# Optimization experiments

Hardware: AMD Instinct MI355X
Metric: run time of the kernel (lower is better)

Reference implementation:

```python
import jax, jax.numpy as jnp
import numpy as np

B, L, A, D = 4, 512, 8, 256
H = 256  # hidden_dim
O = 256  # output_dim


def setup_inputs() -> dict:
    key = jax.random.key(0)
    ks = jax.random.split(key, 12)
    s = 0.05
    return {
        "x": jax.random.normal(ks[0], (B, L, A, D), dtype=jnp.float32),
        "conv_w": jax.random.normal(ks[1], (H, D), dtype=jnp.float32) * s,
        "conv_b": jax.random.normal(ks[2], (H,), dtype=jnp.float32) * s,
        "theta_w": jax.random.normal(ks[3], (H, H), dtype=jnp.float32) * s,
        "theta_b": jax.random.normal(ks[4], (H,), dtype=jnp.float32) * s,
        "phi_w": jax.random.normal(ks[5], (H, H), dtype=jnp.float32) * s,
        "phi_b": jax.random.normal(ks[6], (H,), dtype=jnp.float32) * s,
        "g_w": jax.random.normal(ks[7], (H, H), dtype=jnp.float32) * s,
        "g_b": jax.random.normal(ks[8], (H,), dtype=jnp.float32) * s,
        "f_w": jax.random.normal(ks[9], (O, H), dtype=jnp.float32) * s,
        "f_b": jax.random.normal(ks[10], (O,), dtype=jnp.float32) * s,
    }


def reference(x, conv_w, conv_b, theta_w, theta_b, phi_w, phi_b, g_w, g_b, f_w, f_b):
    batch, length, n_agents, _ = x.shape
    # residual: identity (input_dim == output_dim, stride 1)
    res = x
    # conv with kernel (1,1): pointwise projection over channel dim
    h = jnp.einsum('blad,hd->blah', x, conv_w) + conv_b  # [B,L,A,H]
    N = length * n_agents
    h = h.reshape(batch, N, H)
    theta = jnp.einsum('bnh,kh->bnk', h, theta_w) + theta_b  # [B,N,H]
    phi = jnp.einsum('bnh,kh->bnk', h, phi_w) + phi_b        # [B,N,H]
    g = jnp.einsum('bnh,kh->bnk', h, g_w) + g_b              # [B,N,H]
    scores = jnp.einsum('bnk,bmk->bnm', theta, phi) / jnp.sqrt(jnp.asarray(H, theta.dtype))
    y = jax.nn.softmax(scores, axis=2)                       # [B,N,N]
    z = jnp.einsum('bnm,bmk->bnk', y, g) / jnp.sqrt(jnp.asarray(N, y.dtype))
    out = jnp.einsum('bnk,ok->bno', z, f_w) + f_b            # [B,N,O]
    out = out.reshape(batch, length, n_agents, O)
    return out + res
```

## Files before the change

kernel.cpp:

```cpp
#include <hip/hip_runtime.h>

typedef unsigned short u16;
typedef __bf16 bf16x8 __attribute__((ext_vector_type(8)));
typedef float f32x4 __attribute__((ext_vector_type(4)));
typedef float f32x16 __attribute__((ext_vector_type(16)));
typedef float float4v __attribute__((ext_vector_type(4)));
typedef unsigned short u16x8 __attribute__((ext_vector_type(8)));
typedef unsigned short u16x4 __attribute__((ext_vector_type(4)));

#define MFMA16(a, b, c) __builtin_amdgcn_mfma_f32_16x16x32_bf16(a, b, c, 0, 0, 0)
#define MFMA32(a, b, c) __builtin_amdgcn_mfma_f32_32x32x16_bf16(a, b, c, 0, 0, 0)

__device__ __forceinline__ u16 f2bf(float f) {
  union { float f; unsigned u; } v; v.f = f;
  unsigned r = v.u + 0x7fffu + ((v.u >> 16) & 1u);
  return (u16)(r >> 16);
}
__device__ __forceinline__ float bf2f(u16 b) {
  union { unsigned u; float f; } v; v.u = ((unsigned)b) << 16;
  return v.f;
}

__device__ __forceinline__ void gload16(const void* g, void* l) {
  __builtin_amdgcn_global_load_lds(
      (__attribute__((address_space(1))) void*)g,
      (__attribute__((address_space(3))) void*)l, 16, 0, 0);
}

__device__ __forceinline__ unsigned cvtpk(float lo, float hi) {
  unsigned r;
  asm("v_cvt_pk_bf16_f32 %0, %1, %2" : "=v"(r) : "v"(lo), "v"(hi));
  return r;
}
__device__ __forceinline__ void plswap(unsigned& a, unsigned& b) {
  asm volatile("v_permlane32_swap_b32 %0, %1" : "+v"(a), "+v"(b));
}

__global__ __launch_bounds__(256) void prep_all(
    const float* __restrict__ cw, const float* __restrict__ tw,
    const float* __restrict__ pw, const float* __restrict__ gw,
    const float* __restrict__ fw,
    const float* __restrict__ cb, const float* __restrict__ tb,
    const float* __restrict__ pb, const float* __restrict__ gb,
    u16* __restrict__ Wbig, float* __restrict__ biasp) {
  const int t = threadIdx.x;
  const int bid = blockIdx.x;
  const int n3 = bid & 255;
  __shared__ float w3s[256];
  __shared__ float us[256];
  __shared__ float red[4];
  float pv;
  if (bid < 512) {
    const float* wsrc = bid < 256 ? tw : pw;
    w3s[t] = wsrc[(size_t)n3 * 256 + t];
    __syncthreads();
    float acc = 0.0f;
#pragma unroll 8
    for (int h = 0; h < 256; ++h) acc = fmaf(w3s[h], cw[(size_t)h * 256 + t], acc);
    Wbig[(size_t)bid * 256 + t] = f2bf(acc);
    pv = w3s[t] * cb[t];
  } else {
    w3s[t] = fw[(size_t)n3 * 256 + t];
    __syncthreads();
    float u = 0.0f;
#pragma unroll 8
    for (int h = 0; h < 256; ++h) u = fmaf(w3s[h], gw[(size_t)h * 256 + t], u);
    us[t] = u;
    __syncthreads();
    float acc = 0.0f;
#pragma unroll 8
    for (int k = 0; k < 256; ++k) acc = fmaf(us[k], cw[(size_t)k * 256 + t], acc);
    Wbig[(size_t)bid * 256 + t] = f2bf(acc);
    pv = us[t] * cb[t] + w3s[t] * gb[t];
  }
#pragma unroll
  for (int m = 1; m < 64; m <<= 1) pv += __shfl_xor(pv, m, 64);
  if ((t & 63) == 0) red[t >> 6] = pv;
  __syncthreads();
  if (t == 0) {
    float d = red[0] + red[1] + red[2] + red[3];
    biasp[bid] = d + (bid < 256 ? tb[n3] : bid < 512 ? pb[n3] : 0.0f);
  }
}

__global__ __launch_bounds__(256) void gemm_tpg(
    const float* __restrict__ X, const u16* __restrict__ W,
    const float* __restrict__ bias, u16* __restrict__ tpg,
    u16* __restrict__ gT) {
  __shared__ u16 S[16384];
  u16* As = S;
  u16* Bs = S + 8192;
  const int t = threadIdx.x;
  const int lane = t & 63, w = t >> 6;
  const int brow = blockIdx.x * 128, bcol = blockIdx.y * 128;
  const int wr = (w >> 1) * 64, wc = (w & 1) * 64;
  f32x4 acc[4][4];
#pragma unroll
  for (int i = 0; i < 4; ++i)
#pragma unroll
    for (int j = 0; j < 4; ++j)
#pragma unroll
      for (int r = 0; r < 4; ++r) acc[i][j][r] = 0.0f;

  const int sr = t >> 3, sc8 = (t & 7) * 8;
  const u16* gW = W + (size_t)(bcol + sr) * 256 + sc8;
  const int ar = t & 127, ach = t >> 7;
  const float* gX = X + (size_t)(brow + ar) * 256 + ach * 32;

  for (int kt = 0; kt < 256; kt += 64) {
#pragma unroll
    for (int c = 0; c < 4; ++c)
      gload16(gW + (size_t)c * 32 * 256 + kt, &Bs[c * 2048 + t * 8]);
    u16x8 pk[4];
#pragma unroll
    for (int j = 0; j < 4; ++j) {
      float4v v0 = *(const float4v*)(gX + kt + j * 8);
      float4v v1 = *(const float4v*)(gX + kt + j * 8 + 4);
#pragma unroll
      for (int e = 0; e < 4; ++e) { pk[j][e] = f2bf(v0[e]); pk[j][4 + e] = f2bf(v1[e]); }
    }
#pragma unroll
    for (int j = 0; j < 4; ++j) {
      int unit = (ach * 4 + j) ^ (ar & 7);
      *(u16x8*)(&As[ar * 64 + unit * 8]) = pk[j];
    }
    __syncthreads();
#pragma unroll
    for (int kk = 0; kk < 2; ++kk) {
      const int ko = kk * 32 + (lane >> 4) * 8;
      bf16x8 af[4], bfr[4];
#pragma unroll
      for (int i = 0; i < 4; ++i) {
        int R = wr + i * 16 + (lane & 15);
        int unit = (kk * 4 + (lane >> 4)) ^ (R & 7);
        af[i] = *(const bf16x8*)(&As[R * 64 + unit * 8]);
      }
#pragma unroll
      for (int j = 0; j < 4; ++j)
        bfr[j] = *(const bf16x8*)(&Bs[(wc + j * 16 + (lane & 15)) * 64 + ko]);
#pragma unroll
      for (int i = 0; i < 4; ++i)
#pragma unroll
        for (int j = 0; j < 4; ++j)
          acc[i][j] = MFMA16(af[i], bfr[j], acc[i][j]);
    }
    __syncthreads();
  }

  const int r0 = (lane >> 4) * 4, c0 = lane & 15;
  if (blockIdx.y < 4) {
#pragma unroll
    for (int i = 0; i < 4; ++i)
#pragma unroll
      for (int j = 0; j < 4; ++j) {
        const int col = bcol + wc + j * 16 + c0;
        const float bv = bias[col];
#pragma unroll
        for (int r = 0; r < 4; ++r) {
          const size_t o = (size_t)(brow + wr + i * 16 + r0 + r) * 512 + col;
          tpg[o] = f2bf(acc[i][j][r] + bv);
        }
      }
  } else {
    const int vcb = bcol - 512;
    const int b = brow >> 12, n0 = brow & 4095;
#pragma unroll
    for (int h = 0; h < 2; ++h) {
      if (wr == h * 64) {
#pragma unroll
        for (int i = 0; i < 4; ++i)
#pragma unroll
          for (int j = 0; j < 4; ++j) {
            const int col = wc + j * 16 + c0;
            const float bv = bias[bcol + col];
            const int rowl = i * 16 + r0;
            u16x4 ov;
#pragma unroll
            for (int r = 0; r < 4; ++r) ov[r] = f2bf(acc[i][j][r] + bv);
            *(u16x4*)(&S[col * 72 + rowl]) = ov;
          }
      }
      __syncthreads();
#pragma unroll
      for (int k = 0; k < 4; ++k) {
        const int col = k * 32 + (t >> 3);
        const int mch = (t & 7) * 8;
        u16x8 v = *(const u16x8*)(&S[col * 72 + mch]);
        *(u16x8*)(&gT[((size_t)((b << 8) + vcb + col)) * 4096 + n0 + h * 64 + mch]) = v;
      }
      __syncthreads();
    }
  }
}

__global__ __launch_bounds__(256, 2) void flash2(
    const u16* __restrict__ tpg, const u16* __restrict__ gT,
    u16* __restrict__ Zp, u16* __restrict__ Lpb) {
  __shared__ u16 Kl[2][32 * 256];
  __shared__ u16 Vl[2][256 * 32];

  const int t = threadIdx.x;
  const int lane = t & 63, w = t >> 6;
  const int l31 = lane & 31, hi = lane >> 5;
  const int bid = blockIdx.x;
  const int b = bid >> 7;
  const int quarter = (bid >> 5) & 3;
  const int qt = bid & 31;
  const int q0 = qt * 128 + w * 32;
  const int kv0 = quarter * 1024;

  bf16x8 q[16];
  {
    const u16* qp = tpg + (size_t)(b * 4096 + q0 + l31) * 512 + hi * 8;
#pragma unroll
    for (int ks = 0; ks < 16; ++ks) q[ks] = *(const bf16x8*)(qp + ks * 16);
  }

  f32x16 zacc[8];
#pragma unroll
  for (int i = 0; i < 8; ++i)
#pragma unroll
    for (int j = 0; j < 16; ++j) zacc[i][j] = 0.0f;
  float ell = 0.0f;

  const int ksr = t >> 5, ksc = t & 31;

  auto stage = [&](int tile, int bi) {
    const size_t krow0 = (size_t)(b * 4096 + kv0 + tile * 32);
#pragma unroll
    for (int ch = 0; ch < 4; ++ch) {
      int r = ch * 8 + ksr;
      gload16(tpg + (krow0 + r) * 512 + 256 + ((ksc ^ r) * 8), &Kl[bi][ch * 2048 + t * 8]);
    }
#pragma unroll
    for (int ch = 0; ch < 4; ++ch) {
      int u = ch * 256 + t;
      int r = u >> 2, c16 = u & 3;
      gload16(gT + (size_t)(b * 256 + r) * 4096 + kv0 + tile * 32 + ((c16 ^ ((r >> 1) & 3)) * 8),
              &Vl[bi][u * 8]);
    }
  };

  stage(0, 0);
  __syncthreads();

  for (int tile = 0; tile < 32; ++tile) {
    const int cur = tile & 1;
    if (tile + 1 < 32) stage(tile + 1, cur ^ 1);

    f32x16 s;
#pragma unroll
    for (int j = 0; j < 16; ++j) s[j] = 0.0f;
    const u16* kb = &Kl[cur][0];
    __builtin_amdgcn_s_setprio(1);
#pragma unroll
    for (int ks = 0; ks < 16; ++ks) {
      bf16x8 kf = *(const bf16x8*)(kb + l31 * 256 + (((2 * ks + hi) ^ l31) * 8));
      s = MFMA32(kf, q[ks], s);
    }
    __builtin_amdgcn_s_setprio(0);

    bf16x8 pa[2];
#pragma unroll
    for (int half = 0; half < 2; ++half) {
      float p[8];
#pragma unroll
      for (int g = 0; g < 8; ++g) {
        p[g] = __builtin_amdgcn_exp2f(s[half * 8 + g] * 0.09016844f);
        ell += p[g];
      }
      unsigned x0 = cvtpk(p[0], p[1]), y0 = cvtpk(p[4], p[5]);
      unsigned x1 = cvtpk(p[2], p[3]), y1 = cvtpk(p[6], p[7]);
      plswap(x0, y0);
      plswap(x1, y1);
      union { unsigned u[4]; bf16x8 v; } cc;
      cc.u[0] = x0; cc.u[1] = x1; cc.u[2] = y0; cc.u[3] = y1;
      pa[half] = cc.v;
    }

    const u16* vb = &Vl[cur][0];
    __builtin_amdgcn_s_setprio(1);
#pragma unroll
    for (int ks2 = 0; ks2 < 2; ++ks2) {
#pragma unroll
      for (int nt = 0; nt < 8; ++nt) {
        int row = nt * 32 + l31;
        bf16x8 vv = *(const bf16x8*)(vb + row * 32 + (((2 * ks2 + hi) ^ ((row >> 1) & 3)) * 8));
        zacc[nt] = MFMA32(pa[ks2], vv, zacc[nt]);
      }
    }
    __builtin_amdgcn_s_setprio(0);
    __syncthreads();
  }

  ell += __shfl_xor(ell, 32, 64);

#pragma unroll
  for (int g = 0; g < 16; ++g) {
    int r = (g & 3) + 8 * (g >> 2) + 4 * hi;
    size_t rowoff = ((size_t)(quarter * 16384 + b * 4096 + q0 + r)) * 256 + l31;
#pragma unroll
    for (int nt = 0; nt < 8; ++nt) Zp[rowoff + nt * 32] = f2bf(zacc[nt][g]);
  }
  if (lane < 32) Lpb[quarter * 16384 + b * 4096 + q0 + l31] = f2bf(ell);
}

__global__ __launch_bounds__(256) void merge_out(
    const u16* __restrict__ Zp, const u16* __restrict__ Lpb,
    const float* __restrict__ fb, const float* __restrict__ x,
    float* __restrict__ out) {
  const int idx = blockIdx.x * 256 + threadIdx.x;
  const int m = idx >> 5;
  const int c = (idx & 31) * 8;
  const float l = bf2f(Lpb[m]) + bf2f(Lpb[16384 + m]) + bf2f(Lpb[32768 + m]) +
                  bf2f(Lpb[49152 + m]);
  const float inv = 1.0f / (l * 64.0f);
  float acc[8];
#pragma unroll
  for (int j = 0; j < 8; ++j) acc[j] = 0.0f;
#pragma unroll
  for (int qd = 0; qd < 4; ++qd) {
    u16x8 v = *(const u16x8*)(Zp + ((size_t)(qd * 16384) + m) * 256 + c);
#pragma unroll
    for (int j = 0; j < 8; ++j) acc[j] += bf2f(v[j]);
  }
  const float4v fb0 = *(const float4v*)(fb + c);
  const float4v fb1 = *(const float4v*)(fb + c + 4);
  const float4v x0 = *(const float4v*)(x + (size_t)m * 256 + c);
  const float4v x1 = *(const float4v*)(x + (size_t)m * 256 + c + 4);
  float4v o0, o1;
#pragma unroll
  for (int j = 0; j < 4; ++j) {
    o0[j] = acc[j] * inv + fb0[j] + x0[j];
    o1[j] = acc[4 + j] * inv + fb1[j] + x1[j];
  }
  *(float4v*)(out + (size_t)m * 256 + c) = o0;
  *(float4v*)(out + (size_t)m * 256 + c + 4) = o1;
}

extern "C" void kernel_launch(void* const* d_in, const int* in_sizes, int n_in,
                              void* d_out, int out_size, void* d_ws, size_t ws_size,
                              hipStream_t stream) {
  const float* x  = (const float*)d_in[0];
  const float* cw = (const float*)d_in[1];
  const float* cb = (const float*)d_in[2];
  const float* tw = (const float*)d_in[3];
  const float* tb = (const float*)d_in[4];
  const float* pw = (const float*)d_in[5];
  const float* pb = (const float*)d_in[6];
  const float* gw = (const float*)d_in[7];
  const float* gb = (const float*)d_in[8];
  const float* fw = (const float*)d_in[9];
  const float* fb = (const float*)d_in[10];

  char* ws = (char*)d_ws;
  u16*   tpg   = (u16*)(ws);
  u16*   gT    = (u16*)(ws + 16777216);
  u16*   Zp    = (u16*)(ws + 25165824);
  u16*   Lpb   = (u16*)(ws + 58720256);
  u16*   Wbig  = (u16*)(ws + 58851328);
  float* biasp = (float*)(ws + 59244544);

  prep_all<<<768, 256, 0, stream>>>(cw, tw, pw, gw, fw, cb, tb, pb, gb, Wbig, biasp);
  gemm_tpg<<<dim3(128, 6), 256, 0, stream>>>(x, Wbig, biasp, tpg, gT);
  flash2<<<512, 256, 0, stream>>>(tpg, gT, Zp, Lpb);
  merge_out<<<2048, 256, 0, stream>>>(Zp, Lpb, fb, x, (float*)d_out);
}
```

Measured before the change: 212.2 us.

## Pre-convert X to bf16, async-load GEMM A tiles, remap flash blocks, relax waits

X is converted to bf16 once in extra prep_all blocks, so gemm_tpg loads A tiles with global_load_lds like W instead of doing per-thread fp32 loads, conversion and swizzled LDS stores. The A LDS layout loses its XOR swizzle, which may add bank conflicts. flash2 remaps block IDs so blocks that land on the same XCD share batch/quarter data. Its double-buffered pipeline now uses an explicit vmcnt(8) wait plus raw s_barrier instead of __syncthreads, letting the next tile's loads stay in flight while the current one is computed.

```diff
diff --git a/kernel.cpp b/kernel.cpp
--- a/kernel.cpp
+++ b/kernel.cpp
@@ -42,9 +42,19 @@
     const float* __restrict__ fw,
     const float* __restrict__ cb, const float* __restrict__ tb,
     const float* __restrict__ pb, const float* __restrict__ gb,
-    u16* __restrict__ Wbig, float* __restrict__ biasp) {
+    const float* __restrict__ X,
+    u16* __restrict__ Wbig, float* __restrict__ biasp, u16* __restrict__ xb) {
   const int t = threadIdx.x;
   const int bid = blockIdx.x;
+  if (bid >= 768) {
+    const int idx = (bid - 768) * 256 + t;
+    float4v v = *(const float4v*)(X + (size_t)idx * 4);
+    u16x4 o;
+#pragma unroll
+    for (int i = 0; i < 4; ++i) o[i] = f2bf(v[i]);
+    *(u16x4*)(xb + (size_t)idx * 4) = o;
+    return;
+  }
   const int n3 = bid & 255;
   __shared__ float w3s[256];
   __shared__ float us[256];
@@ -84,7 +94,7 @@
 }
 
 __global__ __launch_bounds__(256) void gemm_tpg(
-    const float* __restrict__ X, const u16* __restrict__ W,
+    const u16* __restrict__ A, const u16* __restrict__ W,
     const float* __restrict__ bias, u16* __restrict__ tpg,
     u16* __restrict__ gT) {
   __shared__ u16 S[16384];
@@ -103,26 +113,14 @@
       for (int r = 0; r < 4; ++r) acc[i][j][r] = 0.0f;
 
   const int sr = t >> 3, sc8 = (t & 7) * 8;
+  const u16* gA = A + (size_t)(brow + sr) * 256 + sc8;
   const u16* gW = W + (size_t)(bcol + sr) * 256 + sc8;
-  const int ar = t & 127, ach = t >> 7;
-  const float* gX = X + (size_t)(brow + ar) * 256 + ach * 32;
 
   for (int kt = 0; kt < 256; kt += 64) {
 #pragma unroll
-    for (int c = 0; c < 4; ++c)
+    for (int c = 0; c < 4; ++c) {
+      gload16(gA + (size_t)c * 32 * 256 + kt, &As[c * 2048 + t * 8]);
       gload16(gW + (size_t)c * 32 * 256 + kt, &Bs[c * 2048 + t * 8]);
-    u16x8 pk[4];
-#pragma unroll
-    for (int j = 0; j < 4; ++j) {
-      float4v v0 = *(const float4v*)(gX + kt + j * 8);
-      float4v v1 = *(const float4v*)(gX + kt + j * 8 + 4);
-#pragma unroll
-      for (int e = 0; e < 4; ++e) { pk[j][e] = f2bf(v0[e]); pk[j][4 + e] = f2bf(v1[e]); }
-    }
-#pragma unroll
-    for (int j = 0; j < 4; ++j) {
-      int unit = (ach * 4 + j) ^ (ar & 7);
-      *(u16x8*)(&As[ar * 64 + unit * 8]) = pk[j];
     }
     __syncthreads();
 #pragma unroll
@@ -130,11 +128,8 @@
       const int ko = kk * 32 + (lane >> 4) * 8;
       bf16x8 af[4], bfr[4];
 #pragma unroll
-      for (int i = 0; i < 4; ++i) {
-        int R = wr + i * 16 + (lane & 15);
-        int unit = (kk * 4 + (lane >> 4)) ^ (R & 7);
-        af[i] = *(const bf16x8*)(&As[R * 64 + unit * 8]);
-      }
+      for (int i = 0; i < 4; ++i)
+        af[i] = *(const bf16x8*)(&As[(wr + i * 16 + (lane & 15)) * 64 + ko]);
 #pragma unroll
       for (int j = 0; j < 4; ++j)
         bfr[j] = *(const bf16x8*)(&Bs[(wc + j * 16 + (lane & 15)) * 64 + ko]);
@@ -202,7 +197,7 @@
   const int t = threadIdx.x;
   const int lane = t & 63, w = t >> 6;
   const int l31 = lane & 31, hi = lane >> 5;
-  const int bid = blockIdx.x;
+  const int bid = ((blockIdx.x & 7) << 6) | (blockIdx.x >> 3);
   const int b = bid >> 7;
   const int quarter = (bid >> 5) & 3;
   const int qt = bid & 31;
@@ -246,7 +241,13 @@
 
   for (int tile = 0; tile < 32; ++tile) {
     const int cur = tile & 1;
-    if (tile + 1 < 32) stage(tile + 1, cur ^ 1);
+    if (tile + 1 < 32) {
+      stage(tile + 1, cur ^ 1);
+      asm volatile("s_waitcnt vmcnt(8)" ::: "memory");
+    } else {
+      asm volatile("s_waitcnt vmcnt(0)" ::: "memory");
+    }
+    asm volatile("s_barrier" ::: "memory");
 
     f32x16 s;
 #pragma unroll
@@ -290,7 +291,7 @@
       }
     }
     __builtin_amdgcn_s_setprio(0);
-    __syncthreads();
+    asm volatile("s_barrier" ::: "memory");
   }
 
   ell += __shfl_xor(ell, 32, 64);
@@ -360,9 +361,11 @@
   u16*   Lpb   = (u16*)(ws + 58720256);
   u16*   Wbig  = (u16*)(ws + 58851328);
   float* biasp = (float*)(ws + 59244544);
-
-  prep_all<<<768, 256, 0, stream>>>(cw, tw, pw, gw, fw, cb, tb, pb, gb, Wbig, biasp);
-  gemm_tpg<<<dim3(128, 6), 256, 0, stream>>>(x, Wbig, biasp, tpg, gT);
+  u16*   xb    = (u16*)(ws + 59247616);
+
+  prep_all<<<4864, 256, 0, stream>>>(cw, tw, pw, gw, fw, cb, tb, pb, gb, x,
+                                     Wbig, biasp, xb);
+  gemm_tpg<<<dim3(128, 6), 256, 0, stream>>>(xb, Wbig, biasp, tpg, gT);
   flash2<<<512, 256, 0, stream>>>(tpg, gT, Zp, Lpb);
   merge_out<<<2048, 256, 0, stream>>>(Zp, Lpb, fb, x, (float*)d_out);
 }
```

Result: faster. 207.2 us (-2.4%).
